# Kernel tuning notes

Hardware: AMD Instinct MI355X
Metric: run time of the kernel (lower is better)

## Reference

```python
import jax, jax.numpy as jnp
import numpy as np

H, D = 8, 16
F = H * D              # hidden_dim = 128
L = 2                  # num HGT layers
NS = [50000, 20000, 10000]                     # gene, disease, drug node counts
EDGE_META = [(0, 0), (0, 1), (2, 0), (2, 1)]   # (src_type, dst_type) per edge type
ES = [300000, 150000, 100000, 50000]
OFFS = [0, NS[0], NS[0] + NS[1], NS[0] + NS[1] + NS[2]]
NTOT = OFFS[-1]
R, T = len(EDGE_META), len(NS)
SQRT_D = float(np.sqrt(D))


def setup_inputs() -> dict:
    key = jax.random.key(0)
    ks = jax.random.split(key, 32)
    inp = {}
    inp["x_gene"] = jax.random.normal(ks[0], (NS[0], F), jnp.float32)
    inp["x_disease"] = jax.random.normal(ks[1], (NS[1], F), jnp.float32)
    inp["x_drug"] = jax.random.normal(ks[2], (NS[2], F), jnp.float32)
    inp["Wkqv"] = 0.05 * jax.random.normal(ks[3], (L, T, F, 3 * F), jnp.float32)
    inp["bkqv"] = jnp.zeros((L, T, 3 * F), jnp.float32)
    inp["Ak"] = 0.1 * jax.random.normal(ks[4], (L, R, H, D, D), jnp.float32)
    inp["Av"] = 0.1 * jax.random.normal(ks[5], (L, R, H, D, D), jnp.float32)
    inp["prel"] = jnp.ones((L, R, H), jnp.float32)   # PyG inits p_rel to ones
    inp["Wout"] = 0.05 * jax.random.normal(ks[6], (L, T, F, F), jnp.float32)
    inp["bout"] = jnp.zeros((L, T, F), jnp.float32)
    inp["skip"] = jnp.ones((L, T), jnp.float32)      # PyG inits skip to 1
    names = ["ei_gg", "ei_gd", "ei_rg", "ei_rd"]
    for i, (name, (st, dt), E) in enumerate(zip(names, EDGE_META, ES)):
        src = jax.random.randint(ks[10 + 2 * i], (E,), 0, NS[st], dtype=jnp.int32)
        dst = jax.random.randint(ks[11 + 2 * i], (E,), 0, NS[dt], dtype=jnp.int32)
        inp[name] = jnp.stack([src, dst])
    return inp


def _hgt_layer(xs, eis, Wkqv_l, bkqv_l, Ak_l, Av_l, prel_l, Wout_l, bout_l, skip_l):
    """One PyG-style HGTConv layer over the heterogeneous graph."""
    kqv = [x @ Wkqv_l[t] + bkqv_l[t] for t, x in enumerate(xs)]
    k = [a[:, :F].reshape(-1, H, D) for a in kqv]
    q = [a[:, F:2 * F].reshape(-1, H, D) for a in kqv]
    v = [a[:, 2 * F:].reshape(-1, H, D) for a in kqv]

    alphas, dsts, ves = [], [], []
    for r, (st, dt) in enumerate(EDGE_META):
        src, dst = eis[r][0], eis[r][1]
        # relation-specific per-head transforms applied on source node set
        k_r = jnp.einsum('nhd,hde->nhe', k[st], Ak_l[r])
        v_r = jnp.einsum('nhd,hde->nhe', v[st], Av_l[r])
        ke = k_r[src]                      # [E, H, D]
        ve = v_r[src]                      # [E, H, D]
        qe = q[dt][dst]                    # [E, H, D]
        a = (qe * ke).sum(-1) * prel_l[r] / SQRT_D   # [E, H]
        alphas.append(a)
        dsts.append(dst + OFFS[dt])
        ves.append(ve)
    alpha = jnp.concatenate(alphas, 0)     # [Etot, H]
    dstg = jnp.concatenate(dsts, 0)        # [Etot]
    ve = jnp.concatenate(ves, 0)           # [Etot, H, D]

    # segment softmax over all incoming edges per destination node
    amax = jax.ops.segment_max(alpha, dstg, num_segments=NTOT)
    ex = jnp.exp(alpha - amax[dstg])
    denom = jax.ops.segment_sum(ex, dstg, num_segments=NTOT)
    w = ex / denom[dstg]
    out = jax.ops.segment_sum(ve * w[..., None], dstg, num_segments=NTOT)
    out = out.reshape(NTOT, F)

    new_xs = []
    for t, x in enumerate(xs):
        o_t = out[OFFS[t]:OFFS[t + 1]]
        o = jax.nn.gelu(o_t, approximate=False) @ Wout_l[t] + bout_l[t]
        a_s = jax.nn.sigmoid(skip_l[t])
        new_xs.append(a_s * o + (1.0 - a_s) * x)
    return new_xs


def reference(x_gene, x_disease, x_drug, Wkqv, bkqv, Ak, Av, prel, Wout, bout,
              skip, ei_gg, ei_gd, ei_rg, ei_rd):
    xs = [x_gene, x_disease, x_drug]
    eis = [ei_gg, ei_gd, ei_rg, ei_rd]
    for l in range(L):
        new = _hgt_layer(xs, eis, Wkqv[l], bkqv[l], Ak[l], Av[l], prel[l],
                         Wout[l], bout[l], skip[l])
        # encoder: dropout(relu(conv_out)) + residual; dropout = identity (eval)
        xs = [jax.nn.relu(n) + x for n, x in zip(new, xs)]
    return tuple(xs)
```

## Files before the change

### kernel.cpp

```cpp
#include <hip/hip_runtime.h>


#define NTOT  80000
#define ETOT  600000
#define NSRC  120000
#define SLOTS 128

typedef unsigned short u16;
typedef unsigned int   u32;
typedef __attribute__((ext_vector_type(8))) short short8;
typedef __attribute__((ext_vector_type(4))) float f32x4;

__device__ __forceinline__ u16 f2bf(float f){
  union { float f; u32 i; } v; v.f = f;
  u32 x = v.i;
  return (u16)((x + 0x7fffu + ((x >> 16) & 1u)) >> 16);
}
__device__ __forceinline__ void unp4(uint4 a, float* o){
  union { u32 i; float f; } t;
  t.i = a.x << 16;        o[0]=t.f;  t.i = a.x & 0xffff0000u; o[1]=t.f;
  t.i = a.y << 16;        o[2]=t.f;  t.i = a.y & 0xffff0000u; o[3]=t.f;
  t.i = a.z << 16;        o[4]=t.f;  t.i = a.z & 0xffff0000u; o[5]=t.f;
  t.i = a.w << 16;        o[6]=t.f;  t.i = a.w & 0xffff0000u; o[7]=t.f;
}
__device__ __forceinline__ void load16bf(const u16* p, float* o){
  unp4(*(const uint4*)p, o); unp4(*(const uint4*)(p + 8), o + 8);
}


#define PR0 2560000
#define PR1 (PR0 + 8*32768)
#define PR2 (PR1 + 2*6*16384)
#define PR3 (PR2 + 2048)
#define PR4 (PR3 + ETOT)

__global__ __launch_bounds__(256) void prep_all(
    const float* __restrict__ xg, const float* __restrict__ xd,
    const float* __restrict__ xr, float* __restrict__ X, u16* __restrict__ Xbf,
    const float* __restrict__ Wkqv, const float* __restrict__ bkqv,
    const float* __restrict__ Ak, const float* __restrict__ Av,
    const float* __restrict__ Wout,
    u16* __restrict__ WeffT, u16* __restrict__ WqT, u16* __restrict__ WoutT,
    float* __restrict__ beff,
    const int* __restrict__ e0, const int* __restrict__ e1,
    const int* __restrict__ e2, const int* __restrict__ e3,
    int* __restrict__ cnt, int* __restrict__ elist)
{
  int i = blockIdx.x * 256 + threadIdx.x;
  if (i < PR0){
    const float* src; int off;
    if (i < 1600000)      { src = xg; off = i; }
    else if (i < 2240000) { src = xd; off = i - 1600000; }
    else                  { src = xr; off = i - 2240000; }
    float4 v = ((const float4*)src)[off];
    ((float4*)X)[i] = v;
    uint2 b;
    b.x = (u32)f2bf(v.x) | ((u32)f2bf(v.y) << 16);
    b.y = (u32)f2bf(v.z) | ((u32)f2bf(v.w) << 16);
    ((uint2*)Xbf)[i] = b;
    return;
  }
  if (i < PR1){
    int j = i - PR0;
    int lr = j >> 15, rem = j & 32767, n = rem >> 7, k = rem & 127;
    int l = lr >> 2, r = lr & 3;
    int st = (r >= 2) ? 2 : 0;
    const float* W = Wkqv + (size_t)(l*3 + st) * 49152;
    float acc = 0.f;
    if (n < 128){
      int h = n >> 4, e = n & 15;
      const float* Am = Ak + (size_t)(l*4 + r) * 2048 + h*256;
#pragma unroll
      for (int d = 0; d < 16; d++) acc += W[k*384 + h*16 + d] * Am[d*16 + e];
    } else {
      int n2 = n - 128, h = n2 >> 4, e = n2 & 15;
      const float* Am = Av + (size_t)(l*4 + r) * 2048 + h*256;
#pragma unroll
      for (int d = 0; d < 16; d++) acc += W[k*384 + 256 + h*16 + d] * Am[d*16 + e];
    }
    WeffT[j] = f2bf(acc);
    return;
  }
  if (i < PR2){
    int j = i - PR1;
    if (j < 6*16384){
      int lt = j >> 14, rem = j & 16383, n = rem >> 7, k = rem & 127;
      WqT[j] = f2bf(Wkqv[(size_t)lt*49152 + k*384 + 128 + n]);
    } else {
      int j2 = j - 6*16384;
      int lt = j2 >> 14, rem = j2 & 16383, n = rem >> 7, k = rem & 127;
      WoutT[j2] = f2bf(Wout[(size_t)lt*16384 + k*128 + n]);
    }
    return;
  }
  if (i < PR3){
    int m = i - PR2;
    int lr = m >> 8, jj = m & 255;
    int l = lr >> 2, r = lr & 3;
    int st = (r >= 2) ? 2 : 0;
    const float* b = bkqv + (size_t)(l*3 + st) * 384;
    float acc = 0.f;
    if (jj < 128){
      int h = jj >> 4, e = jj & 15;
      const float* Am = Ak + (size_t)(l*4 + r) * 2048 + h*256;
#pragma unroll
      for (int d = 0; d < 16; d++) acc += b[h*16 + d] * Am[d*16 + e];
    } else {
      int j2 = jj - 128, h = j2 >> 4, e = j2 & 15;
      const float* Am = Av + (size_t)(l*4 + r) * 2048 + h*256;
#pragma unroll
      for (int d = 0; d < 16; d++) acc += b[256 + h*16 + d] * Am[d*16 + e];
    }
    beff[lr * 256 + jj] = acc;
    return;
  }
  if (i < PR4){
    int e = i - PR3;
    const int* ei; int E, loc, offd, rnoff, rel;
    if (e < 300000)      { ei = e0; E = 300000; loc = e;          offd = 0;     rnoff = 0;      rel = 0; }
    else if (e < 450000) { ei = e1; E = 150000; loc = e - 300000; offd = 50000; rnoff = 50000;  rel = 1; }
    else if (e < 550000) { ei = e2; E = 100000; loc = e - 450000; offd = 0;     rnoff = 100000; rel = 2; }
    else                 { ei = e3; E = 50000;  loc = e - 550000; offd = 50000; rnoff = 110000; rel = 3; }
    int src = ei[loc], dst = ei[E + loc];
    int dstg = offd + dst;
    int pos = atomicAdd(&cnt[dstg], 1);
    if (pos < SLOTS) elist[dstg*SLOTS + pos] = ((rnoff + src) << 2) | rel;
  }
}


__device__ __forceinline__ void stage_bt(const u16* __restrict__ src, u16* BTl){
  int tid = threadIdx.x;
  const uint4* g = (const uint4*)src;
  uint4 tmp[8];
#pragma unroll
  for (int i = 0; i < 8; i++) tmp[i] = g[tid + i*256];
#pragma unroll
  for (int i = 0; i < 8; i++){
    int L = (tid + i*256) * 16;
    int Ls = L ^ (((L >> 8) & 7) << 4);
    *(uint4*)((char*)BTl + Ls) = tmp[i];
  }
}

__device__ __forceinline__ void do_tile(
    const u16* __restrict__ BTsrc, const float* __restrict__ bias,
    u16* __restrict__ C, int ldc, int bm, int M, const short8 af[4], u16* BTl)
{
  stage_bt(BTsrc, BTl);
  __syncthreads();
  int tid = threadIdx.x;
  int lane = tid & 63, w = tid >> 6;
  int quad = lane >> 4, lm = lane & 15;
  f32x4 acc[8];
#pragma unroll
  for (int nt = 0; nt < 8; nt++) acc[nt] = (f32x4){0.f,0.f,0.f,0.f};
#pragma unroll
  for (int nt = 0; nt < 8; nt++){
    int rowb = nt*16 + lm;
    int base = rowb*256 + quad*16;
    int sw = (rowb & 7) << 4;
#pragma unroll
    for (int c = 0; c < 4; c++){
      short8 bf = *(const short8*)((const char*)BTl + ((base + c*64) ^ sw));
      acc[nt] = __builtin_amdgcn_mfma_f32_16x16x32_bf16(af[c], bf, acc[nt], 0, 0, 0);
    }
  }
  __syncthreads();
#pragma unroll
  for (int nt = 0; nt < 8; nt++){
    int col = nt*16 + lm;
    float bb = bias[col];
#pragma unroll
    for (int i = 0; i < 4; i++){
      int r = bm + w*16 + quad*4 + i;
      if (r < M) C[(size_t)r*ldc + col] = f2bf(acc[nt][i] + bb);
    }
  }
}

__global__ __launch_bounds__(256) void mfma_gemm_qkv(
    const u16* __restrict__ Xbf,
    const u16* __restrict__ WqTl, const float* __restrict__ bl,
    const u16* __restrict__ WeffTl, const float* __restrict__ beffl,
    u16* __restrict__ qg, u16* __restrict__ kv)
{
  __shared__ u16 BTl[16384];
  int by = blockIdx.x;
  int t, bm, M, roff, rbase, o0, o1; bool haskv;
  if (by < 782)      { t = 0; bm = by*64;        M = 50000; roff = 0;     haskv = true;  rbase = 0; o0 = 0;      o1 = 50000; }
  else if (by < 939) { t = 2; bm = (by-782)*64;  M = 10000; roff = 70000; haskv = true;  rbase = 2; o0 = 100000; o1 = 110000; }
  else               { t = 1; bm = (by-939)*64;  M = 20000; roff = 50000; haskv = false; rbase = 0; o0 = 0;      o1 = 0; }

  int tid = threadIdx.x;
  int lane = tid & 63, w = tid >> 6;
  int quad = lane >> 4, lm = lane & 15;
  int row = bm + w*16 + lm;
  short8 af[4];
  if (row < M){
    const u16* ap = Xbf + (size_t)(roff + row)*128 + quad*8;
#pragma unroll
    for (int c = 0; c < 4; c++) af[c] = *(const short8*)(ap + c*32);
  } else {
    short8 z = {0,0,0,0,0,0,0,0};
#pragma unroll
    for (int c = 0; c < 4; c++) af[c] = z;
  }

  do_tile(WqTl + (size_t)t*16384, bl + (size_t)t*384 + 128,
          qg + (size_t)roff*128, 128, bm, M, af, BTl);
  if (haskv){
#pragma unroll 1
    for (int s = 0; s < 4; s++){
      int r  = rbase + (s >> 1);
      int bn = (s & 1) * 128;
      int oo = (s < 2) ? o0 : o1;
      do_tile(WeffTl + (size_t)r*32768 + (size_t)bn*128,
              beffl + (size_t)r*256 + bn,
              kv + (size_t)oo*256 + bn, 256, bm, M, af, BTl);
    }
  }
}


__global__ __launch_bounds__(256) void attn_out(
    const u16* __restrict__ qg,
    const u16* __restrict__ kv,
    const float* __restrict__ prel,
    const int* __restrict__ cnt,
    const int* __restrict__ elist,
    const u16* __restrict__ WoutTl,
    const float* __restrict__ bl,
    const float* __restrict__ skipl,
    float* __restrict__ Xall, u16* __restrict__ Xbfall)
{
  __shared__ u16 G[2048];
  int bid = blockIdx.x;
  int t, bm, roff;
  if (bid < 3125)      { t = 0; bm = bid*16;        roff = 0; }
  else if (bid < 4375) { t = 1; bm = (bid-3125)*16; roff = 50000; }
  else                 { t = 2; bm = (bid-4375)*16; roff = 70000; }

  int tid = threadIdx.x;
  int slot = tid >> 4;
  int n = roff + bm + slot;
  int lane = tid & 63;
  int sub = (lane >> 3) & 1;
  int h = lane & 7;
  float sc0 = prel[0*8+h]*0.25f, sc1 = prel[1*8+h]*0.25f,
        sc2 = prel[2*8+h]*0.25f, sc3 = prel[3*8+h]*0.25f;
  float q[16];
  load16bf(qg + (size_t)n * 128 + h*16, q);
  float acc[16] = {};
  float dsum = 0.f;
  int start = n * SLOTS, c = cnt[n];
  if (c > SLOTS) c = SLOTS;

  auto edge = [&](int ev, uint4 ka, uint4 kb, uint4 va, uint4 vb){
    float ke[16], ve[16];
    unp4(ka, ke); unp4(kb, ke + 8);
    unp4(va, ve); unp4(vb, ve + 8);
    float a = 0.f;
#pragma unroll
    for (int d = 0; d < 16; d++) a += q[d] * ke[d];
    int r = ev & 3;
    float s = (r == 0) ? sc0 : (r == 1) ? sc1 : (r == 2) ? sc2 : sc3;
    float ex = expf(a * s);
    dsum += ex;
#pragma unroll
    for (int d = 0; d < 16; d++) acc[d] += ex * ve[d];
  };

  int idx = sub;
#pragma unroll 1
  for (; idx + 6 < c; idx += 8){
    int e0 = elist[start + idx + 0], e1 = elist[start + idx + 2],
        e2 = elist[start + idx + 4], e3 = elist[start + idx + 6];
    const u16* p0 = kv + (size_t)(e0 >> 2) * 256 + h*16;
    const u16* p1 = kv + (size_t)(e1 >> 2) * 256 + h*16;
    const u16* p2 = kv + (size_t)(e2 >> 2) * 256 + h*16;
    const u16* p3 = kv + (size_t)(e3 >> 2) * 256 + h*16;
    uint4 k0a = *(const uint4*)p0,         k0b = *(const uint4*)(p0 + 8);
    uint4 k1a = *(const uint4*)p1,         k1b = *(const uint4*)(p1 + 8);
    uint4 k2a = *(const uint4*)p2,         k2b = *(const uint4*)(p2 + 8);
    uint4 k3a = *(const uint4*)p3,         k3b = *(const uint4*)(p3 + 8);
    uint4 v0a = *(const uint4*)(p0 + 128), v0b = *(const uint4*)(p0 + 136);
    uint4 v1a = *(const uint4*)(p1 + 128), v1b = *(const uint4*)(p1 + 136);
    uint4 v2a = *(const uint4*)(p2 + 128), v2b = *(const uint4*)(p2 + 136);
    uint4 v3a = *(const uint4*)(p3 + 128), v3b = *(const uint4*)(p3 + 136);
    edge(e0, k0a, k0b, v0a, v0b);
    edge(e1, k1a, k1b, v1a, v1b);
    edge(e2, k2a, k2b, v2a, v2b);
    edge(e3, k3a, k3b, v3a, v3b);
  }
#pragma unroll 1
  for (; idx < c; idx += 2){
    int ev = elist[start + idx];
    const u16* p = kv + (size_t)(ev >> 2) * 256 + h*16;
    uint4 ka = *(const uint4*)p,         kb = *(const uint4*)(p + 8);
    uint4 va = *(const uint4*)(p + 128), vb = *(const uint4*)(p + 136);
    edge(ev, ka, kb, va, vb);
  }

  int w = tid >> 6;
  int quad = lane >> 4, lm = lane & 15;
  short8 wf[2][4];
  {
    const u16* wp = WoutTl + (size_t)t*16384;
#pragma unroll
    for (int nt = 0; nt < 2; nt++){
      const u16* wr = wp + (size_t)(w*32 + nt*16 + lm)*128 + quad*8;
#pragma unroll
      for (int c2 = 0; c2 < 4; c2++) wf[nt][c2] = *(const short8*)(wr + c2*32);
    }
  }

  dsum += __shfl_xor(dsum, 8);
#pragma unroll
  for (int d = 0; d < 16; d++) acc[d] += __shfl_xor(acc[d], 8);

  if (sub == 0){
    float inv = (c > 0) ? 1.f / dsum : 0.f;
    u16 o[16];
#pragma unroll
    for (int d = 0; d < 16; d++){
      float x = acc[d] * inv;
      o[d] = f2bf(0.5f * x * (1.f + erff(x * 0.70710678118654752f)));
    }
    uint4 p0, p1;
    p0.x = o[0]|(o[1]<<16);   p0.y = o[2]|(o[3]<<16);
    p0.z = o[4]|(o[5]<<16);   p0.w = o[6]|(o[7]<<16);
    p1.x = o[8]|(o[9]<<16);   p1.y = o[10]|(o[11]<<16);
    p1.z = o[12]|(o[13]<<16); p1.w = o[14]|(o[15]<<16);
    int b0 = slot*256 + h*32;
    int sw = (slot & 7) << 4;
    *(uint4*)((char*)G + (b0 ^ sw))        = p0;
    *(uint4*)((char*)G + ((b0 + 16) ^ sw)) = p1;
  }
  __syncthreads();

  short8 af[4];
  {
    int base = lm*256 + quad*16;
    int sw = (lm & 7) << 4;
#pragma unroll
    for (int c2 = 0; c2 < 4; c2++)
      af[c2] = *(const short8*)((const char*)G + ((base + c2*64) ^ sw));
  }
  f32x4 oacc[2];
#pragma unroll
  for (int nt = 0; nt < 2; nt++){
    oacc[nt] = (f32x4){0.f,0.f,0.f,0.f};
#pragma unroll
    for (int c2 = 0; c2 < 4; c2++)
      oacc[nt] = __builtin_amdgcn_mfma_f32_16x16x32_bf16(af[c2], wf[nt][c2], oacc[nt], 0, 0, 0);
  }
  float a_s = 1.f / (1.f + expf(-skipl[t]));
  float b_s = 1.f - a_s;
  const float* bias = bl + (size_t)t*128;
  float* X = Xall + (size_t)roff*128;
  u16* Xb = Xbfall ? (Xbfall + (size_t)roff*128) : (u16*)0;
#pragma unroll
  for (int nt = 0; nt < 2; nt++){
    int col = w*32 + nt*16 + lm;
    float bb = bias[col];
#pragma unroll
    for (int i = 0; i < 4; i++){
      int r = bm + quad*4 + i;
      float* xp = X + (size_t)r*128 + col;
      float x = *xp;
      float o = oacc[nt][i] + bb;
      float xn = fmaxf(a_s*o + b_s*x, 0.f) + x;
      *xp = xn;
      if (Xb) Xb[(size_t)r*128 + col] = f2bf(xn);
    }
  }
}


extern "C" void kernel_launch(void* const* d_in, const int* in_sizes, int n_in,
                              void* d_out, int out_size, void* d_ws, size_t ws_size,
                              hipStream_t stream)
{
  const float* xg   = (const float*)d_in[0];
  const float* xd   = (const float*)d_in[1];
  const float* xr_  = (const float*)d_in[2];
  const float* Wkqv = (const float*)d_in[3];
  const float* bkqv = (const float*)d_in[4];
  const float* Ak   = (const float*)d_in[5];
  const float* Av   = (const float*)d_in[6];
  const float* prel = (const float*)d_in[7];
  const float* Wout = (const float*)d_in[8];
  const float* bout = (const float*)d_in[9];
  const float* skip = (const float*)d_in[10];
  const int* ei[4] = {(const int*)d_in[11], (const int*)d_in[12],
                      (const int*)d_in[13], (const int*)d_in[14]};

  float* X = (float*)d_out;

  char* p = (char*)d_ws;
  auto alloc = [&](size_t b)->void*{ void* r = (void*)p; p += (b + 255) & ~(size_t)255; return r; };
  int*   cnt   = (int*)  alloc((size_t)NTOT * 4);
  int*   elist = (int*)  alloc((size_t)NTOT * SLOTS * 4);
  float* beff  = (float*)alloc((size_t)8 * 256 * 4);
  u16*   qg    = (u16*)  alloc((size_t)NTOT * 128 * 2);
  u16*   kv    = (u16*)  alloc((size_t)NSRC * 256 * 2);
  u16*   Xbf   = (u16*)  alloc((size_t)NTOT * 128 * 2);
  u16*   WqT   = (u16*)  alloc((size_t)6 * 16384 * 2);
  u16*   WeffT = (u16*)  alloc((size_t)8 * 32768 * 2);
  u16*   WoutT = (u16*)  alloc((size_t)6 * 16384 * 2);
  (void)ws_size; (void)in_sizes; (void)n_in; (void)out_size;

  hipMemsetAsync(cnt, 0, (size_t)NTOT * 4, stream);

  prep_all<<<(PR4 + 255)/256, 256, 0, stream>>>(
      xg, xd, xr_, X, Xbf,
      Wkqv, bkqv, Ak, Av, Wout, WeffT, WqT, WoutT, beff,
      ei[0], ei[1], ei[2], ei[3], cnt, elist);

  for (int l = 0; l < 2; l++){
    mfma_gemm_qkv<<<1252, 256, 0, stream>>>(
        Xbf,
        WqT + (size_t)l*3*16384, bkqv + (size_t)l*3*384,
        WeffT + (size_t)l*4*32768, beff + (size_t)l*4*256,
        qg, kv);
    attn_out<<<5000, 256, 0, stream>>>(
        qg, kv, prel + l*32, cnt, elist,
        WoutT + (size_t)l*3*16384, bout + (size_t)l*3*128, skip + l*3,
        X, (l == 0) ? Xbf : (u16*)0);
  }
}
```

Measured before the change: 396.4 us.

## Split QKV GEMM blocks per relation and prefetch next weight tile into registers

The QKV/relation GEMM kernel now launches separate blocks per relation, so each block handles at most three output tiles instead of five. This raises the block count and balances work across blocks. Inside a block, the next weight tile is loaded from global memory into registers while the current tile is computed, then written to shared memory after the barrier. The trade-off is that A fragments are reloaded by more blocks and register pressure rises from holding the prefetch buffer.

```diff
diff --git a/kernel.cpp b/kernel.cpp
--- a/kernel.cpp
+++ b/kernel.cpp
@@ -129,26 +129,24 @@
 }
 
 
-__device__ __forceinline__ void stage_bt(const u16* __restrict__ src, u16* BTl){
-  int tid = threadIdx.x;
+__device__ __forceinline__ void bt_load(const u16* __restrict__ src, uint4* tmp){
   const uint4* g = (const uint4*)src;
-  uint4 tmp[8];
-#pragma unroll
-  for (int i = 0; i < 8; i++) tmp[i] = g[tid + i*256];
+#pragma unroll
+  for (int i = 0; i < 8; i++) tmp[i] = g[threadIdx.x + i*256];
+}
+__device__ __forceinline__ void bt_write(const uint4* tmp, u16* BTl){
 #pragma unroll
   for (int i = 0; i < 8; i++){
-    int L = (tid + i*256) * 16;
+    int L = (threadIdx.x + i*256) * 16;
     int Ls = L ^ (((L >> 8) & 7) << 4);
     *(uint4*)((char*)BTl + Ls) = tmp[i];
   }
 }
 
-__device__ __forceinline__ void do_tile(
-    const u16* __restrict__ BTsrc, const float* __restrict__ bias,
-    u16* __restrict__ C, int ldc, int bm, int M, const short8 af[4], u16* BTl)
+__device__ __forceinline__ void tile_compute(
+    const u16* BTl, const short8 af[4], const float* __restrict__ bias,
+    u16* __restrict__ C, int ldc, int bm, int M)
 {
-  stage_bt(BTsrc, BTl);
-  __syncthreads();
   int tid = threadIdx.x;
   int lane = tid & 63, w = tid >> 6;
   int quad = lane >> 4, lm = lane & 15;
@@ -166,7 +164,6 @@
       acc[nt] = __builtin_amdgcn_mfma_f32_16x16x32_bf16(af[c], bf, acc[nt], 0, 0, 0);
     }
   }
-  __syncthreads();
 #pragma unroll
   for (int nt = 0; nt < 8; nt++){
     int col = nt*16 + lm;
@@ -187,10 +184,12 @@
 {
   __shared__ u16 BTl[16384];
   int by = blockIdx.x;
-  int t, bm, M, roff, rbase, o0, o1; bool haskv;
-  if (by < 782)      { t = 0; bm = by*64;        M = 50000; roff = 0;     haskv = true;  rbase = 0; o0 = 0;      o1 = 50000; }
-  else if (by < 939) { t = 2; bm = (by-782)*64;  M = 10000; roff = 70000; haskv = true;  rbase = 2; o0 = 100000; o1 = 110000; }
-  else               { t = 1; bm = (by-939)*64;  M = 20000; roff = 50000; haskv = false; rbase = 0; o0 = 0;      o1 = 0; }
+  int t, bm, M, roff, rW, ooff; bool hasq, haspair;
+  if (by < 782)       { t = 0; bm = by*64;         M = 50000; roff = 0;     hasq = true;  haspair = true;  rW = 0; ooff = 0; }
+  else if (by < 1564) { t = 0; bm = (by-782)*64;   M = 50000; roff = 0;     hasq = false; haspair = true;  rW = 1; ooff = 50000; }
+  else if (by < 1721) { t = 2; bm = (by-1564)*64;  M = 10000; roff = 70000; hasq = true;  haspair = true;  rW = 2; ooff = 100000; }
+  else if (by < 1878) { t = 2; bm = (by-1721)*64;  M = 10000; roff = 70000; hasq = false; haspair = true;  rW = 3; ooff = 110000; }
+  else                { t = 1; bm = (by-1878)*64;  M = 20000; roff = 50000; hasq = true;  haspair = false; rW = 0; ooff = 0; }
 
   int tid = threadIdx.x;
   int lane = tid & 63, w = tid >> 6;
@@ -207,18 +206,34 @@
     for (int c = 0; c < 4; c++) af[c] = z;
   }
 
-  do_tile(WqTl + (size_t)t*16384, bl + (size_t)t*384 + 128,
-          qg + (size_t)roff*128, 128, bm, M, af, BTl);
-  if (haskv){
+  const u16* qW   = WqTl + (size_t)t*16384;
+  const u16* pW   = WeffTl + (size_t)rW*32768;
+  const float* qb = bl + (size_t)t*384 + 128;
+  const float* pb = beffl + (size_t)rW*256;
+  u16* qC = qg + (size_t)roff*128;
+  u16* pC = kv + (size_t)ooff*256;
+
+  int base_ti = hasq ? 0 : 1;
+  int ntile = (hasq ? 1 : 0) + (haspair ? 2 : 0);
+
+  uint4 tmp[8];
+  bt_load(base_ti == 0 ? qW : pW, tmp);
+  bt_write(tmp, BTl);
 #pragma unroll 1
-    for (int s = 0; s < 4; s++){
-      int r  = rbase + (s >> 1);
-      int bn = (s & 1) * 128;
-      int oo = (s < 2) ? o0 : o1;
-      do_tile(WeffTl + (size_t)r*32768 + (size_t)bn*128,
-              beffl + (size_t)r*256 + bn,
-              kv + (size_t)oo*256 + bn, 256, bm, M, af, BTl);
-    }
+  for (int s = 0; s < ntile; s++){
+    bool more = (s + 1 < ntile);
+    if (more){
+      int tin = base_ti + s + 1;
+      bt_load((tin == 1) ? pW : pW + 16384, tmp);
+    }
+    __syncthreads();
+    int ti = base_ti + s;
+    const float* bias = (ti == 0) ? qb : (ti == 1 ? pb : pb + 128);
+    u16* C            = (ti == 0) ? qC : (ti == 1 ? pC : pC + 128);
+    int ldc           = (ti == 0) ? 128 : 256;
+    tile_compute(BTl, af, bias, C, ldc, bm, M);
+    __syncthreads();
+    if (more) bt_write(tmp, BTl);
   }
 }
 
@@ -419,7 +434,7 @@
       ei[0], ei[1], ei[2], ei[3], cnt, elist);
 
   for (int l = 0; l < 2; l++){
-    mfma_gemm_qkv<<<1252, 256, 0, stream>>>(
+    mfma_gemm_qkv<<<2191, 256, 0, stream>>>(
         Xbf,
         WqT + (size_t)l*3*16384, bkqv + (size_t)l*3*384,
         WeffT + (size_t)l*4*32768, beff + (size_t)l*4*256,
```

Result: slower. 475.4 us (+19.9%).
